# Optimization experiments

Hardware: AMD Instinct MI355X
Metric: run time of the kernel (lower is better)

## Reference

```python
import jax, jax.numpy as jnp
import numpy as np

EMBED = 1024
DMODEL = 1024
NHEAD = 16
HEAD = DMODEL // NHEAD  # 64
EPS = 1e-5


def layer_norm(x, g, b):
    mu = jnp.mean(x, axis=-1, keepdims=True)
    var = jnp.var(x, axis=-1, keepdims=True)
    return (x - mu) / jnp.sqrt(var + EPS) * g + b


def setup_inputs() -> dict:
    key = jax.random.key(0)
    ks = jax.random.split(key, 16)
    s = 0.02
    B, T = 2, 2048
    return {
        "x": jax.random.normal(ks[0], (B, T, EMBED), jnp.float32),
        "wq": jax.random.normal(ks[1], (NHEAD, EMBED, HEAD), jnp.float32) * s,
        "bq": jnp.zeros((NHEAD, HEAD), jnp.float32),
        "wk": jax.random.normal(ks[2], (NHEAD, EMBED, HEAD), jnp.float32) * s,
        "bk": jnp.zeros((NHEAD, HEAD), jnp.float32),
        "wv": jax.random.normal(ks[3], (NHEAD, EMBED, HEAD), jnp.float32) * s,
        "bv": jnp.zeros((NHEAD, HEAD), jnp.float32),
        "ln1_g": jnp.ones((EMBED,), jnp.float32),
        "ln1_b": jnp.zeros((EMBED,), jnp.float32),
        "ln2_g": jnp.ones((DMODEL,), jnp.float32),
        "ln2_b": jnp.zeros((DMODEL,), jnp.float32),
        "w1": jax.random.normal(ks[4], (DMODEL, 4 * DMODEL), jnp.float32) * s,
        "b1": jnp.zeros((4 * DMODEL,), jnp.float32),
        "w2": jax.random.normal(ks[5], (4 * DMODEL, EMBED), jnp.float32) * s,
        "b2": jnp.zeros((EMBED,), jnp.float32),
    }


def reference(x, wq, bq, wk, bk, wv, bv, ln1_g, ln1_b, ln2_g, ln2_b, w1, b1, w2, b2):
    B, T, C = x.shape
    h = layer_norm(x, ln1_g, ln1_b)  # note: residual uses the normalized x (as in source)
    # per-head projections, vectorized over heads: [B,H,T,D]
    q = jnp.einsum('btc,hcd->bhtd', h, wq) + bq[None, :, None, :]
    k = jnp.einsum('btc,hcd->bhtd', h, wk) + bk[None, :, None, :]
    v = jnp.einsum('btc,hcd->bhtd', h, wv) + bv[None, :, None, :]
    scores = jnp.einsum('bhtd,bhsd->bhts', q, k) / jnp.sqrt(jnp.float32(HEAD))
    causal = jnp.tril(jnp.ones((T, T), bool))
    scores = jnp.where(causal[None, None], scores, jnp.finfo(scores.dtype).min)
    wei = jax.nn.softmax(scores, axis=-1)
    attn = jnp.einsum('bhts,bhsd->bhtd', wei, v)
    attn = attn.transpose(0, 2, 1, 3).reshape(B, T, NHEAD * HEAD)  # concat heads
    y = h + attn
    z = layer_norm(y, ln2_g, ln2_b)
    ff = jax.nn.relu(z @ w1 + b1) @ w2 + b2
    return z + ff
```

## Files before the change

kernel.cpp:

```cpp
#include <hip/hip_runtime.h>
#include <hip/hip_bf16.h>
#include <cstdint>
#include <cstddef>

typedef __attribute__((ext_vector_type(8))) short bf16x8;
typedef __attribute__((ext_vector_type(4))) float f32x4;
typedef __attribute__((ext_vector_type(4))) short short4v;
typedef __attribute__((ext_vector_type(2))) unsigned int uint2v;

__device__ inline void gload_lds16(const void* g, void* l) {
  __builtin_amdgcn_global_load_lds((const __attribute__((address_space(1))) void*)g,
                                   (__attribute__((address_space(3))) void*)l, 16, 0, 0);
}

__device__ inline float exp2_fast(float x) {
  float r;
  asm volatile("v_exp_f32 %0, %1" : "=v"(r) : "v"(x));
  return r;
}

__device__ inline unsigned int cvt_pk_bf16(float lo, float hi) {
  unsigned int r;
  asm volatile("v_cvt_pk_bf16_f32 %0, %1, %2" : "=v"(r) : "v"(lo), "v"(hi));
  return r;
}

__device__ inline float bf2f(short s) {
  return __uint_as_float(((unsigned int)(unsigned short)s) << 16);
}

__global__ void transpose_pack(const float* __restrict__ src, __hip_bfloat16* __restrict__ dst,
                               int R, int C, int ldDst, long zSrcStride, int zDstRow)
{
  __shared__ float tile[64][65];
  src += (size_t)blockIdx.z * zSrcStride;
  const int r0 = blockIdx.y * 64, c0 = blockIdx.x * 64;
  const int t = threadIdx.x;
#pragma unroll
  for (int i = 0; i < 16; ++i) {
    int idx = i * 256 + t;
    int r = idx >> 6, c = idx & 63;
    tile[r][c] = src[(size_t)(r0 + r) * C + c0 + c];
  }
  __syncthreads();
  const int drow0 = blockIdx.z * zDstRow + c0;
#pragma unroll
  for (int i = 0; i < 16; ++i) {
    int idx = i * 256 + t;
    int cc = idx >> 6, rr = idx & 63;
    dst[(size_t)(drow0 + cc) * ldDst + r0 + rr] = __float2bfloat16(tile[rr][cc]);
  }
}

__global__ void ln_fused(const float* __restrict__ x,
                         const float* __restrict__ g, const float* __restrict__ bta,
                         float* __restrict__ of32, __hip_bfloat16* __restrict__ obf)
{
  const int row = blockIdx.x;
  const int t = threadIdx.x;
  float4 v = ((const float4*)(x + (size_t)row * 1024))[t];
  float s = v.x + v.y + v.z + v.w;
  float ss = v.x * v.x + v.y * v.y + v.z * v.z + v.w * v.w;
#pragma unroll
  for (int off = 1; off < 64; off <<= 1) {
    s += __shfl_xor(s, off);
    ss += __shfl_xor(ss, off);
  }
  __shared__ float sb[4], ssb[4];
  const int w = t >> 6, lane = t & 63;
  if (lane == 0) { sb[w] = s; ssb[w] = ss; }
  __syncthreads();
  s = sb[0] + sb[1] + sb[2] + sb[3];
  ss = ssb[0] + ssb[1] + ssb[2] + ssb[3];
  const float mu = s * (1.f / 1024.f);
  const float var = ss * (1.f / 1024.f) - mu * mu;
  const float rstd = rsqrtf(var + 1e-5f);
  float4 gv = ((const float4*)g)[t];
  float4 bv = ((const float4*)bta)[t];
  float4 o;
  o.x = (v.x - mu) * rstd * gv.x + bv.x;
  o.y = (v.y - mu) * rstd * gv.y + bv.y;
  o.z = (v.z - mu) * rstd * gv.z + bv.z;
  o.w = (v.w - mu) * rstd * gv.w + bv.w;
  ((float4*)(of32 + (size_t)row * 1024))[t] = o;
  __hip_bfloat16 hb[4] = { __float2bfloat16(o.x), __float2bfloat16(o.y),
                           __float2bfloat16(o.z), __float2bfloat16(o.w) };
  *(short4v*)(obf + (size_t)row * 1024 + t * 4) = *(const short4v*)hb;
}

__global__ void ln2_merge_fused(const float* __restrict__ hres,
                                const __hip_bfloat16* __restrict__ Opart,
                                const float* __restrict__ Lpart,
                                const float* __restrict__ g, const float* __restrict__ bta,
                                float* __restrict__ of32, __hip_bfloat16* __restrict__ obf)
{
  const int row = blockIdx.x;
  const int b = row >> 11, tt = row & 2047;
  const int qblk = tt >> 7, qloc = tt & 127;
  const int nch = (qblk >> 2) + 1;
  const int t = threadIdx.x;
  const int hd = t >> 4;
  const int d0 = (t & 15) * 4;
  const int base = ((b * 16 + hd) * 16 + qblk) << 2;

  float4 v = ((const float4*)(hres + (size_t)row * 1024))[t];
  float l = 0.f;
  float o0 = 0.f, o1 = 0.f, o2 = 0.f, o3 = 0.f;
  for (int ch = 0; ch < nch; ++ch) {
    l += Lpart[(size_t)(base + ch) * 128 + qloc];
    short4v o4 = *(const short4v*)(Opart + (size_t)(base + ch) * 8192 + qloc * 64 + d0);
    o0 += bf2f(o4[0]); o1 += bf2f(o4[1]); o2 += bf2f(o4[2]); o3 += bf2f(o4[3]);
  }
  const float inv = 1.f / l;
  v.x += o0 * inv; v.y += o1 * inv; v.z += o2 * inv; v.w += o3 * inv;

  float s = v.x + v.y + v.z + v.w;
  float ss = v.x * v.x + v.y * v.y + v.z * v.z + v.w * v.w;
#pragma unroll
  for (int off = 1; off < 64; off <<= 1) {
    s += __shfl_xor(s, off);
    ss += __shfl_xor(ss, off);
  }
  __shared__ float sb[4], ssb[4];
  const int w = t >> 6, lane = t & 63;
  if (lane == 0) { sb[w] = s; ssb[w] = ss; }
  __syncthreads();
  s = sb[0] + sb[1] + sb[2] + sb[3];
  ss = ssb[0] + ssb[1] + ssb[2] + ssb[3];
  const float mu = s * (1.f / 1024.f);
  const float var = ss * (1.f / 1024.f) - mu * mu;
  const float rstd = rsqrtf(var + 1e-5f);
  float4 gv = ((const float4*)g)[t];
  float4 bv = ((const float4*)bta)[t];
  float4 o;
  o.x = (v.x - mu) * rstd * gv.x + bv.x;
  o.y = (v.y - mu) * rstd * gv.y + bv.y;
  o.z = (v.z - mu) * rstd * gv.z + bv.z;
  o.w = (v.w - mu) * rstd * gv.w + bv.w;
  ((float4*)(of32 + (size_t)row * 1024))[t] = o;
  __hip_bfloat16 hb[4] = { __float2bfloat16(o.x), __float2bfloat16(o.y),
                           __float2bfloat16(o.z), __float2bfloat16(o.w) };
  *(short4v*)(obf + (size_t)row * 1024 + t * 4) = *(const short4v*)hb;
}

template<int EPI>
__global__ __launch_bounds__(512, 2) void gemm_bt(
    const __hip_bfloat16* __restrict__ A, const __hip_bfloat16* __restrict__ Bt,
    int N, int Kf, int kLen,
    const float* __restrict__ bias,
    const float* __restrict__ bq, const float* __restrict__ bk, const float* __restrict__ bv,
    __hip_bfloat16* __restrict__ oq, __hip_bfloat16* __restrict__ ok, __hip_bfloat16* __restrict__ ovt,
    __hip_bfloat16* __restrict__ obf,
    float* __restrict__ opart0, float* __restrict__ opart1, float* __restrict__ opart2)
{
  __shared__ short As[2][128 * 32];
  __shared__ short Bs[2][256 * 32];
  const int t = threadIdx.x;
  const int lane = t & 63;
  const int w = t >> 6;
  const int wm = w >> 2, wn = w & 3;
  const int l15 = lane & 15, lg = lane >> 4;
  const int m0 = blockIdx.y * 128;
  const int n0 = blockIdx.x * 256;
  const int kBase = (EPI == 2) ? (int)blockIdx.z * kLen : 0;
  const int kEnd0 = kBase + kLen;
  const int kEnd = (kEnd0 > Kf) ? Kf : kEnd0;

  f32x4 acc[4][4];
#pragma unroll
  for (int i = 0; i < 4; ++i)
#pragma unroll
    for (int j = 0; j < 4; ++j)
#pragma unroll
      for (int e = 0; e < 4; ++e) acc[i][j][e] = 0.f;

  auto STAGE = [&](int buf, int kk0) {
    {
      const int r = t >> 2, cc = t & 3;
      const int kk = (cc ^ ((r >> 1) & 3)) * 8;
      gload_lds16(A + (size_t)(m0 + r) * Kf + kk0 + kk, (char*)As + buf * 8192 + t * 16);
    }
#pragma unroll
    for (int i = 0; i < 2; ++i) {
      const int c = t + 512 * i;
      const int r = c >> 2, cc = c & 3;
      const int kk = (cc ^ ((r >> 1) & 3)) * 8;
      gload_lds16(Bt + (size_t)(n0 + r) * Kf + kk0 + kk, (char*)Bs + buf * 16384 + c * 16);
    }
  };

  STAGE(0, kBase);
  int buf = 0;
  for (int k0 = kBase; k0 < kEnd; k0 += 32) {
    const int knext = (k0 + 32 < kEnd) ? k0 + 32 : k0;
    STAGE(buf ^ 1, knext);
    asm volatile("s_waitcnt vmcnt(3)" ::: "memory");
    __builtin_amdgcn_s_barrier();
    asm volatile("" ::: "memory");

    bf16x8 af[4], bfr[4];
#pragma unroll
    for (int fm = 0; fm < 4; ++fm) {
      const int r = wm * 64 + fm * 16 + l15;
      const int kc = lg ^ ((r >> 1) & 3);
      af[fm] = *(const bf16x8*)&As[buf][r * 32 + kc * 8];
    }
#pragma unroll
    for (int fn = 0; fn < 4; ++fn) {
      const int r = wn * 64 + fn * 16 + l15;
      const int kc = lg ^ ((r >> 1) & 3);
      bfr[fn] = *(const bf16x8*)&Bs[buf][r * 32 + kc * 8];
    }
#pragma unroll
    for (int fm = 0; fm < 4; ++fm)
#pragma unroll
      for (int fn = 0; fn < 4; ++fn)
        acc[fm][fn] = __builtin_amdgcn_mfma_f32_16x16x32_bf16(af[fm], bfr[fn], acc[fm][fn], 0, 0, 0);

    asm volatile("" ::: "memory");
    __builtin_amdgcn_s_barrier();
    buf ^= 1;
  }

#pragma unroll
  for (int fm = 0; fm < 4; ++fm) {
    const int mbase = m0 + wm * 64 + fm * 16 + lg * 4;
#pragma unroll
    for (int fn = 0; fn < 4; ++fn) {
      const int n = n0 + wn * 64 + fn * 16 + l15;
      if (EPI == 0) {
        const int seg = n >> 10;
        const int cn = n & 1023;
        const int h = cn >> 6, d = cn & 63;
        const float* bp = (seg == 0) ? bq : (seg == 1) ? bk : bv;
        const float bias_v = bp[cn];
#pragma unroll
        for (int rg = 0; rg < 4; ++rg) {
          const int m = mbase + rg;
          const int b = m >> 11, tt = m & 2047;
          const size_t bh = (size_t)(b * 16 + h);
          const float val = acc[fm][fn][rg] + bias_v;
          if (seg == 0)      oq[(bh * 2048 + tt) * 64 + d] = __float2bfloat16(val);
          else if (seg == 1) ok[(bh * 2048 + tt) * 64 + d] = __float2bfloat16(val);
          else               ovt[(bh * 64 + d) * 2048 + tt] = __float2bfloat16(val);
        }
      } else if (EPI == 1) {
        const float bias_v = bias[n];
#pragma unroll
        for (int rg = 0; rg < 4; ++rg) {
          const int m = mbase + rg;
          float val = acc[fm][fn][rg] + bias_v;
          val = fmaxf(val, 0.f);
          obf[(size_t)m * N + n] = __float2bfloat16(val);
        }
      } else {
        float* op = (blockIdx.z == 0) ? opart0 : (blockIdx.z == 1) ? opart1 : opart2;
#pragma unroll
        for (int rg = 0; rg < 4; ++rg) {
          const int m = mbase + rg;
          op[(size_t)m * 1024 + n] = acc[fm][fn][rg];
        }
      }
    }
  }
}

__global__ void ffn2_merge(const float* __restrict__ p0, const float* __restrict__ p1,
                           const float* __restrict__ p2,
                           const float* __restrict__ z, const float* __restrict__ b2,
                           float* __restrict__ out)
{
  const size_t i = ((size_t)blockIdx.x * 256 + threadIdx.x) * 4;
  const float4 a = *(const float4*)(p0 + i);
  const float4 b = *(const float4*)(p1 + i);
  const float4 d = *(const float4*)(p2 + i);
  const float4 c = *(const float4*)(z + i);
  const float4 bb = *(const float4*)(b2 + (i & 1023));
  float4 o;
  o.x = c.x + bb.x + a.x + b.x + d.x;
  o.y = c.y + bb.y + a.y + b.y + d.y;
  o.z = c.z + bb.z + a.z + b.z + d.z;
  o.w = c.w + bb.w + a.w + b.w + d.w;
  *(float4*)(out + i) = o;
}

__global__ __launch_bounds__(256, 3) void flash_attn(
    const __hip_bfloat16* __restrict__ Q, const __hip_bfloat16* __restrict__ Kb,
    const __hip_bfloat16* __restrict__ Vt,
    __hip_bfloat16* __restrict__ Opart, float* __restrict__ Lpart)
{
  __shared__ short Ks[2][64 * 64];
  __shared__ short Vs[2][64 * 64];
  __shared__ short P2[4][32 * 72];
  const int t = threadIdx.x;
  const int lane = t & 63, w = t >> 6;
  const int l15 = lane & 15, lg = lane >> 4;
  const int chunk = blockIdx.x, qblk = blockIdx.y, bh = blockIdx.z;
  const int q0 = qblk * 128;
  const int s_base = chunk * 512;
  if (s_base > q0 + 127) return;
  const int s_hi = (s_base + 512 < q0 + 128) ? s_base + 512 : q0 + 128;
  const int ntiles = (s_hi - s_base) >> 6;
  const int qw = q0 + w * 32;

  const __hip_bfloat16* Qbh = Q + (size_t)bh * 2048 * 64;
  const __hip_bfloat16* Kbh = Kb + (size_t)bh * 2048 * 64;
  const __hip_bfloat16* Vbh = Vt + (size_t)bh * 64 * 2048;

  bf16x8 qf[2][2];
#pragma unroll
  for (int fm = 0; fm < 2; ++fm)
#pragma unroll
    for (int kc = 0; kc < 2; ++kc)
      qf[fm][kc] = *(const bf16x8*)(Qbh + (size_t)(qw + fm * 16 + l15) * 64 + kc * 32 + lg * 8);

  const int srow = (w << 4) + (lane >> 3);
  const int schunk = ((lane & 7) ^ (lane >> 3)) * 8;

  auto STAGE = [&](int bufi, int s0) {
#pragma unroll
    for (int i = 0; i < 2; ++i) {
      const int r = srow + i * 8;
      const int dst = bufi * 8192 + w * 2048 + i * 1024 + lane * 16;
      gload_lds16(Kbh + (size_t)(s0 + r) * 64 + schunk, (char*)Ks + dst);
      gload_lds16(Vbh + (size_t)r * 2048 + s0 + schunk, (char*)Vs + dst);
    }
  };

  f32x4 o_acc[2][4];
  float lpart[2] = {0.f, 0.f};
#pragma unroll
  for (int fm = 0; fm < 2; ++fm)
#pragma unroll
    for (int fd = 0; fd < 4; ++fd)
#pragma unroll
      for (int e = 0; e < 4; ++e) o_acc[fm][fd][e] = 0.f;

  const float C = 0.18033688011112042f;

  STAGE(0, s_base);
  int cur = 0;
  for (int ti = 0; ti < ntiles; ++ti) {
    const int s0 = s_base + ti * 64;
    const int nxt = (ti + 1 < ntiles) ? s0 + 64 : s0;
    STAGE(cur ^ 1, nxt);
    asm volatile("s_waitcnt vmcnt(4)" ::: "memory");
    __builtin_amdgcn_s_barrier();
    asm volatile("" ::: "memory");

    if (s0 <= qw + 31) {
      f32x4 s_acc[2][4];
#pragma unroll
      for (int fm = 0; fm < 2; ++fm)
#pragma unroll
        for (int fn = 0; fn < 4; ++fn)
#pragma unroll
          for (int e = 0; e < 4; ++e) s_acc[fm][fn][e] = 0.f;
#pragma unroll
      for (int kc = 0; kc < 2; ++kc)
#pragma unroll
        for (int fn = 0; fn < 4; ++fn) {
          const int r = fn * 16 + l15;
          bf16x8 kf = *(const bf16x8*)&Ks[cur][r * 64 + ((((kc << 2) | lg) ^ (l15 & 7)) << 3)];
          s_acc[0][fn] = __builtin_amdgcn_mfma_f32_16x16x32_bf16(kf, qf[0][kc], s_acc[0][fn], 0, 0, 0);
          s_acc[1][fn] = __builtin_amdgcn_mfma_f32_16x16x32_bf16(kf, qf[1][kc], s_acc[1][fn], 0, 0, 0);
        }

      const bool needmask = (s0 + 63 > qw);
      float pr[2][4][4];
#pragma unroll
      for (int fm = 0; fm < 2; ++fm) {
        const int qv = qw + fm * 16 + l15;
#pragma unroll
        for (int fn = 0; fn < 4; ++fn)
#pragma unroll
          for (int rg = 0; rg < 4; ++rg) {
            float p = exp2_fast(s_acc[fm][fn][rg] * C);
            if (needmask) {
              const int sg = s0 + fn * 16 + lg * 4 + rg;
              p = (sg <= qv) ? p : 0.f;
            }
            pr[fm][fn][rg] = p;
            lpart[fm] += p;
          }
      }

#pragma unroll
      for (int fm = 0; fm < 2; ++fm)
#pragma unroll
        for (int fn = 0; fn < 4; ++fn) {
          uint2v u;
          u.x = cvt_pk_bf16(pr[fm][fn][0], pr[fm][fn][1]);
          u.y = cvt_pk_bf16(pr[fm][fn][2], pr[fm][fn][3]);
          *(uint2v*)&P2[w][(fm * 16 + l15) * 72 + fn * 16 + lg * 4] = u;
        }

#pragma unroll
      for (int kc = 0; kc < 2; ++kc) {
        bf16x8 pf0 = *(const bf16x8*)&P2[w][(l15) * 72 + kc * 32 + lg * 8];
        bf16x8 pf1 = *(const bf16x8*)&P2[w][(16 + l15) * 72 + kc * 32 + lg * 8];
#pragma unroll
        for (int fd = 0; fd < 4; ++fd) {
          const int r = fd * 16 + l15;
          bf16x8 vf = *(const bf16x8*)&Vs[cur][r * 64 + ((((kc << 2) | lg) ^ (l15 & 7)) << 3)];
          o_acc[0][fd] = __builtin_amdgcn_mfma_f32_16x16x32_bf16(vf, pf0, o_acc[0][fd], 0, 0, 0);
          o_acc[1][fd] = __builtin_amdgcn_mfma_f32_16x16x32_bf16(vf, pf1, o_acc[1][fd], 0, 0, 0);
        }
      }
    }

    asm volatile("" ::: "memory");
    __builtin_amdgcn_s_barrier();
    cur ^= 1;
  }

  const int pslot = ((bh * 16 + qblk) << 2) + chunk;
  __hip_bfloat16* op = Opart + (size_t)pslot * 8192;
#pragma unroll
  for (int fm = 0; fm < 2; ++fm) {
    float l = lpart[fm];
    l += __shfl_xor(l, 16);
    l += __shfl_xor(l, 32);
    const int qloc = w * 32 + fm * 16 + l15;
    if (lg == 0) Lpart[pslot * 128 + qloc] = l;
#pragma unroll
    for (int fd = 0; fd < 4; ++fd) {
      uint2v u;
      u.x = cvt_pk_bf16(o_acc[fm][fd][0], o_acc[fm][fd][1]);
      u.y = cvt_pk_bf16(o_acc[fm][fd][2], o_acc[fm][fd][3]);
      *(uint2v*)(op + (size_t)qloc * 64 + fd * 16 + lg * 4) = u;
    }
  }
}

extern "C" void kernel_launch(void* const* d_in, const int* in_sizes, int n_in,
                              void* d_out, int out_size, void* d_ws, size_t ws_size,
                              hipStream_t stream) {
  const float* x    = (const float*)d_in[0];
  const float* wq   = (const float*)d_in[1];
  const float* bq   = (const float*)d_in[2];
  const float* wk   = (const float*)d_in[3];
  const float* bk   = (const float*)d_in[4];
  const float* wv   = (const float*)d_in[5];
  const float* bv   = (const float*)d_in[6];
  const float* ln1g = (const float*)d_in[7];
  const float* ln1b = (const float*)d_in[8];
  const float* ln2g = (const float*)d_in[9];
  const float* ln2b = (const float*)d_in[10];
  const float* w1   = (const float*)d_in[11];
  const float* b1   = (const float*)d_in[12];
  const float* w2   = (const float*)d_in[13];
  const float* b2   = (const float*)d_in[14];
  float* out = (float*)d_out;

  char* ws = (char*)d_ws;
  const size_t MB = 1024 * 1024;
  __hip_bfloat16* h_bf  = (__hip_bfloat16*)(ws + 0);
  float* z_f32          = (float*)(ws + 0);
  __hip_bfloat16* qb    = (__hip_bfloat16*)(ws + 8 * MB);
  __hip_bfloat16* kb    = (__hip_bfloat16*)(ws + 16 * MB);
  __hip_bfloat16* z_bf  = (__hip_bfloat16*)(ws + 16 * MB);
  __hip_bfloat16* vtb   = (__hip_bfloat16*)(ws + 24 * MB);
  __hip_bfloat16* ff1   = (__hip_bfloat16*)(ws + 24 * MB);
  float* h_f32          = (float*)(ws + 32 * MB);
  __hip_bfloat16* Opart = (__hip_bfloat16*)(ws + 48 * MB);
  float* p0             = (float*)(ws + 56 * MB);
  float* p1             = (float*)(ws + 72 * MB);
  float* Lpart          = (float*)(ws + 80 * MB);
  __hip_bfloat16* wqkvT = (__hip_bfloat16*)(ws + 88 * MB);
  float* p2             = (float*)(ws + 88 * MB);
  __hip_bfloat16* w1T   = (__hip_bfloat16*)(ws + 96 * MB);
  __hip_bfloat16* w2T   = (__hip_bfloat16*)(ws + 104 * MB);

  transpose_pack<<<dim3(1, 16, 16), 256, 0, stream>>>(wq, wqkvT + 0 * 1024 * 1024, 1024, 64, 1024, 65536, 64);
  transpose_pack<<<dim3(1, 16, 16), 256, 0, stream>>>(wk, wqkvT + 1 * 1024 * 1024, 1024, 64, 1024, 65536, 64);
  transpose_pack<<<dim3(1, 16, 16), 256, 0, stream>>>(wv, wqkvT + 2 * 1024 * 1024, 1024, 64, 1024, 65536, 64);
  transpose_pack<<<dim3(64, 16, 1), 256, 0, stream>>>(w1, w1T, 1024, 4096, 1024, 0, 0);
  transpose_pack<<<dim3(16, 64, 1), 256, 0, stream>>>(w2, w2T, 4096, 1024, 4096, 0, 0);

  ln_fused<<<4096, 256, 0, stream>>>(x, ln1g, ln1b, h_f32, h_bf);

  gemm_bt<0><<<dim3(12, 32), 512, 0, stream>>>(h_bf, wqkvT, 3072, 1024, 1024,
      nullptr, bq, bk, bv, qb, kb, vtb, nullptr, nullptr, nullptr, nullptr);

  flash_attn<<<dim3(4, 16, 32), 256, 0, stream>>>(qb, kb, vtb, Opart, Lpart);

  ln2_merge_fused<<<4096, 256, 0, stream>>>(h_f32, Opart, Lpart, ln2g, ln2b, z_f32, z_bf);

  gemm_bt<1><<<dim3(16, 32), 512, 0, stream>>>(z_bf, w1T, 4096, 1024, 1024,
      b1, nullptr, nullptr, nullptr, nullptr, nullptr, nullptr, ff1, nullptr, nullptr, nullptr);

  gemm_bt<2><<<dim3(4, 32, 3), 512, 0, stream>>>(ff1, w2T, 1024, 4096, 1376,
      nullptr, nullptr, nullptr, nullptr, nullptr, nullptr, nullptr, nullptr, p0, p1, p2);

  ffn2_merge<<<4096, 256, 0, stream>>>(p0, p1, p2, z_f32, b2, out);
}
```

Measured before the change: 245.1 us.

## Load K/V tiles directly into registers per wave and drop LDS staging and barriers

The flash attention kernel no longer stages K and V tiles through block-shared LDS with async global-to-LDS loads and two block barriers per tile. Each wave now loads its K and V MFMA fragments straight from global memory into two register buffers, prefetching the next tile while it computes the current one. Waves leave the loop independently once past their causal limit. The cost is that all four waves fetch the same K/V data (more global/L2 traffic) and register pressure rises, which is why the occupancy hint drops from 3 to 2 blocks. The prefetch after the last tile of a chunk can also read past the chunk range.

```diff
diff --git a/kernel.cpp b/kernel.cpp
--- a/kernel.cpp
+++ b/kernel.cpp
@@ -284,13 +284,11 @@
   *(float4*)(out + i) = o;
 }
 
-__global__ __launch_bounds__(256, 3) void flash_attn(
+__global__ __launch_bounds__(256, 2) void flash_attn(
     const __hip_bfloat16* __restrict__ Q, const __hip_bfloat16* __restrict__ Kb,
     const __hip_bfloat16* __restrict__ Vt,
     __hip_bfloat16* __restrict__ Opart, float* __restrict__ Lpart)
 {
-  __shared__ short Ks[2][64 * 64];
-  __shared__ short Vs[2][64 * 64];
   __shared__ short P2[4][32 * 72];
   const int t = threadIdx.x;
   const int lane = t & 63, w = t >> 6;
@@ -314,17 +312,21 @@
     for (int kc = 0; kc < 2; ++kc)
       qf[fm][kc] = *(const bf16x8*)(Qbh + (size_t)(qw + fm * 16 + l15) * 64 + kc * 32 + lg * 8);
 
-  const int srow = (w << 4) + (lane >> 3);
-  const int schunk = ((lane & 7) ^ (lane >> 3)) * 8;
-
-  auto STAGE = [&](int bufi, int s0) {
-#pragma unroll
-    for (int i = 0; i < 2; ++i) {
-      const int r = srow + i * 8;
-      const int dst = bufi * 8192 + w * 2048 + i * 1024 + lane * 16;
-      gload_lds16(Kbh + (size_t)(s0 + r) * 64 + schunk, (char*)Ks + dst);
-      gload_lds16(Vbh + (size_t)r * 2048 + s0 + schunk, (char*)Vs + dst);
-    }
+  bf16x8 kA[2][4], vA[2][4], kB[2][4], vB[2][4];
+
+  auto LOADK = [&](bf16x8 (&kf)[2][4], int s0) {
+#pragma unroll
+    for (int kc = 0; kc < 2; ++kc)
+#pragma unroll
+      for (int fn = 0; fn < 4; ++fn)
+        kf[kc][fn] = *(const bf16x8*)(Kbh + (size_t)(s0 + fn * 16 + l15) * 64 + kc * 32 + lg * 8);
+  };
+  auto LOADV = [&](bf16x8 (&vf)[2][4], int s0) {
+#pragma unroll
+    for (int kc = 0; kc < 2; ++kc)
+#pragma unroll
+      for (int fd = 0; fd < 4; ++fd)
+        vf[kc][fd] = *(const bf16x8*)(Vbh + (size_t)(fd * 16 + l15) * 2048 + s0 + kc * 32 + lg * 8);
   };
 
   f32x4 o_acc[2][4];
@@ -338,80 +340,72 @@
 
   const float C = 0.18033688011112042f;
 
-  STAGE(0, s_base);
-  int cur = 0;
-  for (int ti = 0; ti < ntiles; ++ti) {
+  auto TILE = [&](bf16x8 (&kf)[2][4], bf16x8 (&vf)[2][4],
+                  bf16x8 (&kn)[2][4], bf16x8 (&vn)[2][4],
+                  int s0, bool pre) {
+    f32x4 s_acc[2][4];
+#pragma unroll
+    for (int fm = 0; fm < 2; ++fm)
+#pragma unroll
+      for (int fn = 0; fn < 4; ++fn)
+#pragma unroll
+        for (int e = 0; e < 4; ++e) s_acc[fm][fn][e] = 0.f;
+#pragma unroll
+    for (int kc = 0; kc < 2; ++kc)
+#pragma unroll
+      for (int fn = 0; fn < 4; ++fn) {
+        s_acc[0][fn] = __builtin_amdgcn_mfma_f32_16x16x32_bf16(kf[kc][fn], qf[0][kc], s_acc[0][fn], 0, 0, 0);
+        s_acc[1][fn] = __builtin_amdgcn_mfma_f32_16x16x32_bf16(kf[kc][fn], qf[1][kc], s_acc[1][fn], 0, 0, 0);
+      }
+    if (pre) LOADK(kn, s0 + 64);
+
+    const bool needmask = (s0 + 63 > qw);
+#pragma unroll
+    for (int fm = 0; fm < 2; ++fm) {
+      const int qv = qw + fm * 16 + l15;
+#pragma unroll
+      for (int fn = 0; fn < 4; ++fn) {
+        float p[4];
+#pragma unroll
+        for (int rg = 0; rg < 4; ++rg) {
+          float pv = exp2_fast(s_acc[fm][fn][rg] * C);
+          if (needmask) {
+            const int sg = s0 + fn * 16 + lg * 4 + rg;
+            pv = (sg <= qv) ? pv : 0.f;
+          }
+          p[rg] = pv;
+          lpart[fm] += pv;
+        }
+        uint2v u;
+        u.x = cvt_pk_bf16(p[0], p[1]);
+        u.y = cvt_pk_bf16(p[2], p[3]);
+        *(uint2v*)&P2[w][(fm * 16 + l15) * 72 + fn * 16 + lg * 4] = u;
+      }
+    }
+
+#pragma unroll
+    for (int kc = 0; kc < 2; ++kc) {
+      bf16x8 pf0 = *(const bf16x8*)&P2[w][(l15) * 72 + kc * 32 + lg * 8];
+      bf16x8 pf1 = *(const bf16x8*)&P2[w][(16 + l15) * 72 + kc * 32 + lg * 8];
+#pragma unroll
+      for (int fd = 0; fd < 4; ++fd) {
+        o_acc[0][fd] = __builtin_amdgcn_mfma_f32_16x16x32_bf16(vf[kc][fd], pf0, o_acc[0][fd], 0, 0, 0);
+        o_acc[1][fd] = __builtin_amdgcn_mfma_f32_16x16x32_bf16(vf[kc][fd], pf1, o_acc[1][fd], 0, 0, 0);
+      }
+    }
+    if (pre) LOADV(vn, s0 + 64);
+  };
+
+  LOADK(kA, s_base);
+  LOADV(vA, s_base);
+
+  for (int ti = 0; ti < ntiles; ti += 2) {
     const int s0 = s_base + ti * 64;
-    const int nxt = (ti + 1 < ntiles) ? s0 + 64 : s0;
-    STAGE(cur ^ 1, nxt);
-    asm volatile("s_waitcnt vmcnt(4)" ::: "memory");
-    __builtin_amdgcn_s_barrier();
-    asm volatile("" ::: "memory");
-
-    if (s0 <= qw + 31) {
-      f32x4 s_acc[2][4];
-#pragma unroll
-      for (int fm = 0; fm < 2; ++fm)
-#pragma unroll
-        for (int fn = 0; fn < 4; ++fn)
-#pragma unroll
-          for (int e = 0; e < 4; ++e) s_acc[fm][fn][e] = 0.f;
-#pragma unroll
-      for (int kc = 0; kc < 2; ++kc)
-#pragma unroll
-        for (int fn = 0; fn < 4; ++fn) {
-          const int r = fn * 16 + l15;
-          bf16x8 kf = *(const bf16x8*)&Ks[cur][r * 64 + ((((kc << 2) | lg) ^ (l15 & 7)) << 3)];
-          s_acc[0][fn] = __builtin_amdgcn_mfma_f32_16x16x32_bf16(kf, qf[0][kc], s_acc[0][fn], 0, 0, 0);
-          s_acc[1][fn] = __builtin_amdgcn_mfma_f32_16x16x32_bf16(kf, qf[1][kc], s_acc[1][fn], 0, 0, 0);
-        }
-
-      const bool needmask = (s0 + 63 > qw);
-      float pr[2][4][4];
-#pragma unroll
-      for (int fm = 0; fm < 2; ++fm) {
-        const int qv = qw + fm * 16 + l15;
-#pragma unroll
-        for (int fn = 0; fn < 4; ++fn)
-#pragma unroll
-          for (int rg = 0; rg < 4; ++rg) {
-            float p = exp2_fast(s_acc[fm][fn][rg] * C);
-            if (needmask) {
-              const int sg = s0 + fn * 16 + lg * 4 + rg;
-              p = (sg <= qv) ? p : 0.f;
-            }
-            pr[fm][fn][rg] = p;
-            lpart[fm] += p;
-          }
-      }
-
-#pragma unroll
-      for (int fm = 0; fm < 2; ++fm)
-#pragma unroll
-        for (int fn = 0; fn < 4; ++fn) {
-          uint2v u;
-          u.x = cvt_pk_bf16(pr[fm][fn][0], pr[fm][fn][1]);
-          u.y = cvt_pk_bf16(pr[fm][fn][2], pr[fm][fn][3]);
-          *(uint2v*)&P2[w][(fm * 16 + l15) * 72 + fn * 16 + lg * 4] = u;
-        }
-
-#pragma unroll
-      for (int kc = 0; kc < 2; ++kc) {
-        bf16x8 pf0 = *(const bf16x8*)&P2[w][(l15) * 72 + kc * 32 + lg * 8];
-        bf16x8 pf1 = *(const bf16x8*)&P2[w][(16 + l15) * 72 + kc * 32 + lg * 8];
-#pragma unroll
-        for (int fd = 0; fd < 4; ++fd) {
-          const int r = fd * 16 + l15;
-          bf16x8 vf = *(const bf16x8*)&Vs[cur][r * 64 + ((((kc << 2) | lg) ^ (l15 & 7)) << 3)];
-          o_acc[0][fd] = __builtin_amdgcn_mfma_f32_16x16x32_bf16(vf, pf0, o_acc[0][fd], 0, 0, 0);
-          o_acc[1][fd] = __builtin_amdgcn_mfma_f32_16x16x32_bf16(vf, pf1, o_acc[1][fd], 0, 0, 0);
-        }
-      }
-    }
-
-    asm volatile("" ::: "memory");
-    __builtin_amdgcn_s_barrier();
-    cur ^= 1;
+    if (s0 > qw + 31) break;
+    TILE(kA, vA, kB, vB, s0, true);
+    const int s1 = s0 + 64;
+    if (s1 > qw + 31) break;
+    TILE(kB, vB, kA, vA, s1, ti + 2 < ntiles);
   }
 
   const int pslot = ((bh * 16 + qblk) << 2) + chunk;
```

New measurement: 311.6 us. 1.27x slower.
